# Performance work log

Hardware: AMD Instinct MI355X
Metric: run time of the kernel (lower is better)

Reference implementation:

```python
import jax, jax.numpy as jnp
from jax import lax
import numpy as np

S = 2048      # seq_len
E = 1024      # embedding_dim
H = 512       # hidden per direction (hidden_dim // 2)
V = 50000     # vocab
T = 16        # tagset_size
START, STOP = 0, 1
NEG = -10000.0


def setup_inputs() -> dict:
    key = jax.random.key(0)
    ks = jax.random.split(key, 20)
    bound = 1.0 / np.sqrt(H)

    def u(k, shape):
        return jax.random.uniform(k, shape, minval=-bound, maxval=bound, dtype=jnp.float32)

    sentence = jax.random.randint(ks[0], (S,), 0, V)
    emb = jax.random.normal(ks[1], (V, E), dtype=jnp.float32) * 0.1
    # PyTorch LSTM weights, gate order (i, f, g, o) stacked along first dim
    Wih_f = u(ks[2], (4 * H, E)); Whh_f = u(ks[3], (4 * H, H))
    bih_f = u(ks[4], (4 * H,));   bhh_f = u(ks[5], (4 * H,))
    Wih_b = u(ks[6], (4 * H, E)); Whh_b = u(ks[7], (4 * H, H))
    bih_b = u(ks[8], (4 * H,));   bhh_b = u(ks[9], (4 * H,))
    # init_hidden(): randn initial (h0, c0), [2 directions, H] (batch=1 squeezed)
    h0 = jax.random.normal(ks[10], (2, H), dtype=jnp.float32)
    c0 = jax.random.normal(ks[11], (2, H), dtype=jnp.float32)
    Wout = u(ks[12], (T, 2 * H)); bout = u(ks[13], (T,))
    transitions = jax.random.normal(ks[14], (T, T), dtype=jnp.float32)
    transitions = transitions.at[START, :].set(NEG).at[:, STOP].set(NEG)
    return dict(sentence=sentence, emb=emb,
                Wih_f=Wih_f, Whh_f=Whh_f, bih_f=bih_f, bhh_f=bhh_f,
                Wih_b=Wih_b, Whh_b=Whh_b, bih_b=bih_b, bhh_b=bhh_b,
                h0=h0, c0=c0, Wout=Wout, bout=bout, transitions=transitions)


def _lstm_dir(x, Wih, Whh, bih, bhh, h0, c0):
    # x: [S, E] -> hs: [S, H]; PyTorch gate order i, f, g, o
    xg = x @ Wih.T + bih + bhh  # precompute input contribution [S, 4H]

    def step(carry, xg_t):
        h, c = carry
        g = xg_t + h @ Whh.T
        i, f, gg, o = jnp.split(g, 4)
        i, f, o = jax.nn.sigmoid(i), jax.nn.sigmoid(f), jax.nn.sigmoid(o)
        c = f * c + i * jnp.tanh(gg)
        h = o * jnp.tanh(c)
        return (h, c), h

    _, hs = lax.scan(step, (h0, c0), xg)
    return hs


def _feats(sentence, emb, Wih_f, Whh_f, bih_f, bhh_f, Wih_b, Whh_b, bih_b, bhh_b,
           h0, c0, Wout, bout):
    x = emb[sentence]  # [S, E]
    hf = _lstm_dir(x, Wih_f, Whh_f, bih_f, bhh_f, h0[0], c0[0])              # [S, H]
    hb = _lstm_dir(x[::-1], Wih_b, Whh_b, bih_b, bhh_b, h0[1], c0[1])[::-1]  # [S, H]
    out = jnp.concatenate([hf, hb], axis=-1)  # [S, 2H]
    return out @ Wout.T + bout                # [S, T]


def _viterbi(feats, transitions):
    v0 = jnp.full((T,), NEG, dtype=feats.dtype).at[START].set(0.0)

    def vstep(v, feat):
        scores = v[None, :] + transitions        # [T(next), T(prev)]
        bp = jnp.argmax(scores, axis=1)          # best prev tag per next tag
        v_new = jnp.max(scores, axis=1) + feat
        return v_new, bp

    v, bps = lax.scan(vstep, v0, feats)          # bps: [S, T]
    terminal = v + transitions[STOP]
    best = jnp.argmax(terminal)
    path_score = terminal[best]

    def btstep(tag, bp):
        return bp[tag], tag

    _, path = lax.scan(btstep, best, bps, reverse=True)  # path[t] = tag at t
    return path_score, path


def reference(sentence, emb, Wih_f, Whh_f, bih_f, bhh_f, Wih_b, Whh_b, bih_b, bhh_b,
              h0, c0, Wout, bout, transitions):
    feats = _feats(sentence, emb, Wih_f, Whh_f, bih_f, bhh_f,
                   Wih_b, Whh_b, bih_b, bhh_b, h0, c0, Wout, bout)
    path_score, path = _viterbi(feats, transitions)
    return path_score, path
```

## Files before the change

kernel.cpp:

```cpp
#include <hip/hip_runtime.h>
#include <hip/hip_bf16.h>

#define S 2048
#define NEGV -10000.0f

typedef unsigned long long ull;
typedef unsigned int uint4v __attribute__((ext_vector_type(4)));

__device__ __forceinline__ float fsig(float x) {
  return 1.0f / (1.0f + __expf(-x));
}
__device__ __forceinline__ float ftanh(float x) {
  float a = fabsf(x);
  float e = __expf(-2.0f * a);
  float r = (1.0f - e) / (1.0f + e);
  return copysignf(r, x);
}

__global__ void init_k(const float* __restrict__ h0, ull* __restrict__ hbuf,
                       int* __restrict__ flags) {
  int b = blockIdx.x, u = threadIdx.x;
  if (b < 2) {
    ull pk = (1ULL << 32) | (ull)__float_as_uint(h0[b * 512 + u]);
    __hip_atomic_store(&hbuf[b * 1024 + u], pk, __ATOMIC_RELAXED, __HIP_MEMORY_SCOPE_AGENT);
    __hip_atomic_store(&hbuf[b * 1024 + 512 + u], 0ULL, __ATOMIC_RELAXED, __HIP_MEMORY_SCOPE_AGENT);
  } else {
    __hip_atomic_store(&flags[(b - 2) * 512 + u], 0, __ATOMIC_RELAXED, __HIP_MEMORY_SCOPE_AGENT);
    if (b == 2 && u < 2)
      __hip_atomic_store(&flags[2048 + u], 0, __ATOMIC_RELAXED, __HIP_MEMORY_SCOPE_AGENT);
  }
}

__device__ __forceinline__ ull compose_map(ull a, ull b) {
  ull r = 0;
  #pragma unroll
  for (int i = 0; i < 16; ++i) {
    int bi = (int)((b >> (4 * i)) & 15);
    int ai = (int)((a >> (4 * bi)) & 15);
    r |= (ull)ai << (4 * i);
  }
  return r;
}

__device__ __forceinline__ ull spread16(ull x) {
  x &= 0xFFFFULL;
  x = (x | (x << 24)) & 0x000000FF000000FFULL;
  x = (x | (x << 12)) & 0x000F000F000F000FULL;
  x = (x | (x << 6))  & 0x0303030303030303ULL;
  x = (x | (x << 3))  & 0x1111111111111111ULL;
  return x;
}

__global__ __launch_bounds__(256) void fused_k(
    const int* __restrict__ sent, const float* __restrict__ emb,
    const float* __restrict__ Wih_f, const float* __restrict__ Wih_b,
    const float* __restrict__ bih_f, const float* __restrict__ bhh_f,
    const float* __restrict__ bih_b, const float* __restrict__ bhh_b,
    const float* __restrict__ Whh_f, const float* __restrict__ Whh_b,
    const float* __restrict__ c0,
    const float* __restrict__ Wout, const float* __restrict__ bout,
    const float* __restrict__ trans,
    float* __restrict__ xg,
    ull* __restrict__ hbuf,
    float* __restrict__ hs_cat,
    float* __restrict__ feats,
    int* __restrict__ flags,
    float* __restrict__ out)
{
  __shared__ __align__(16) float smem[4544];
  const int t = threadIdx.x;

  if (blockIdx.x >= 128) {
    float* Asm = smem;
    float* Bsm = smem + 2304;
    int*   sidx = (int*)(smem + 4480);
    const int tm = t >> 4, tn = t & 15;
    const int lr = t >> 2, lkq = t & 3;

    for (int i = 0; i < 16; ++i) {
      const int T = (blockIdx.x - 128) + 128 * i;
      const int byo = T >> 6, bxo = T & 63;
      const int by = (byo & 1) ? (31 - (byo >> 1)) : (byo >> 1);
      const int bx = (bxo & 1) ? (32 + (bxo >> 1)) : (bxo >> 1);
      const int n0 = bx * 64, m0 = by * 64;

      const float* W = (n0 < 2048) ? (Wih_f + (size_t)n0 * 1024)
                                   : (Wih_b + (size_t)(n0 - 2048) * 1024);
      __syncthreads();
      if (t < 64) sidx[t] = sent[m0 + t];
      __syncthreads();

      float acc[4][4] = {};
      for (int k0 = 0; k0 < 1024; k0 += 32) {
        const float* ap = emb + (size_t)sidx[lr] * 1024 + k0 + lkq * 8;
        float4 a0 = *(const float4*)ap;
        float4 a1 = *(const float4*)(ap + 4);
        const float* bp = W + (size_t)lr * 1024 + k0 + lkq * 8;
        float4 b0 = *(const float4*)bp;
        float4 b1 = *(const float4*)(bp + 4);
        __syncthreads();
        *(float4*)&Asm[lr * 36 + lkq * 8]     = a0;
        *(float4*)&Asm[lr * 36 + lkq * 8 + 4] = a1;
        {
          const float* bb0 = (const float*)&b0;
          const float* bb1 = (const float*)&b1;
          #pragma unroll
          for (int j = 0; j < 4; ++j) Bsm[(lkq * 8 + j) * 68 + lr] = bb0[j];
          #pragma unroll
          for (int j = 0; j < 4; ++j) Bsm[(lkq * 8 + 4 + j) * 68 + lr] = bb1[j];
        }
        __syncthreads();
        #pragma unroll
        for (int kk = 0; kk < 32; ++kk) {
          float a0_ = Asm[(tm * 4 + 0) * 36 + kk];
          float a1_ = Asm[(tm * 4 + 1) * 36 + kk];
          float a2_ = Asm[(tm * 4 + 2) * 36 + kk];
          float a3_ = Asm[(tm * 4 + 3) * 36 + kk];
          float4 bv = *(const float4*)&Bsm[kk * 68 + tn * 4];
          acc[0][0] = fmaf(a0_, bv.x, acc[0][0]); acc[0][1] = fmaf(a0_, bv.y, acc[0][1]);
          acc[0][2] = fmaf(a0_, bv.z, acc[0][2]); acc[0][3] = fmaf(a0_, bv.w, acc[0][3]);
          acc[1][0] = fmaf(a1_, bv.x, acc[1][0]); acc[1][1] = fmaf(a1_, bv.y, acc[1][1]);
          acc[1][2] = fmaf(a1_, bv.z, acc[1][2]); acc[1][3] = fmaf(a1_, bv.w, acc[1][3]);
          acc[2][0] = fmaf(a2_, bv.x, acc[2][0]); acc[2][1] = fmaf(a2_, bv.y, acc[2][1]);
          acc[2][2] = fmaf(a2_, bv.z, acc[2][2]); acc[2][3] = fmaf(a2_, bv.w, acc[2][3]);
          acc[3][0] = fmaf(a3_, bv.x, acc[3][0]); acc[3][1] = fmaf(a3_, bv.y, acc[3][1]);
          acc[3][2] = fmaf(a3_, bv.z, acc[3][2]); acc[3][3] = fmaf(a3_, bv.w, acc[3][3]);
        }
      }

      const float* bi = (n0 < 2048) ? bih_f : bih_b;
      const float* bh = (n0 < 2048) ? bhh_f : bhh_b;
      const int nb = (n0 < 2048) ? n0 : (n0 - 2048);
      #pragma unroll
      for (int ii = 0; ii < 4; ++ii) {
        int m = m0 + tm * 4 + ii;
        #pragma unroll
        for (int j = 0; j < 4; ++j) {
          int nn = tn * 4 + j;
          float bias = bi[nb + nn] + bh[nb + nn];
          __hip_atomic_store(&xg[(size_t)m * 4096 + n0 + nn], acc[ii][j] + bias,
                             __ATOMIC_RELAXED, __HIP_MEMORY_SCOPE_AGENT);
        }
      }
      asm volatile("s_waitcnt vmcnt(0)" ::: "memory");
      __syncthreads();
      if (t == 0)
        __hip_atomic_store(&flags[by * 64 + bx], 1, __ATOMIC_RELAXED, __HIP_MEMORY_SCOPE_AGENT);
    }
    return;
  }

  {
    const int w = blockIdx.x;
    const int dir = w & 1;
    const int wid = w >> 1;
    const int rr = t >> 3;
    const int seg = t & 7;
    const int g  = rr & 3;
    const int ul = rr >> 2;
    const int unit = wid * 8 + ul;
    const int grow = g * 512 + unit;
    const int bxf  = dir * 32 + g * 8 + (wid >> 3);

    float (*h_lds)[544] = (float(*)[544])smem;

    const float* Whh = dir ? Whh_b : Whh_f;
    float wreg[64];
    {
      const float* src = Whh + (size_t)grow * 512 + seg * 64;
      #pragma unroll
      for (int j = 0; j < 16; ++j) {
        float4 v = *(const float4*)(src + j * 4);
        wreg[4 * j + 0] = v.x; wreg[4 * j + 1] = v.y;
        wreg[4 * j + 2] = v.z; wreg[4 * j + 3] = v.w;
      }
    }

    ull* hb = hbuf + dir * 1024;
    float c_reg = c0[dir * 512 + unit];

    const int u0 = t * 2;
    const int wchunk = u0 >> 6, wpos = u0 & 63;

    float xg_a = 0.0f, xg_b = 0.0f;
    if (seg == 0) {
      int by0 = dir ? 31 : 0;
      while (__hip_atomic_load(&flags[by0 * 64 + bxf], __ATOMIC_RELAXED,
                               __HIP_MEMORY_SCOPE_AGENT) != 1)
        __builtin_amdgcn_s_sleep(8);
      int r0 = dir ? (S - 1) : 0;
      int r1 = dir ? (S - 2) : 1;
      xg_a = __hip_atomic_load(&xg[(size_t)r0 * 4096 + dir * 2048 + grow],
                               __ATOMIC_RELAXED, __HIP_MEMORY_SCOPE_AGENT);
      xg_b = __hip_atomic_load(&xg[(size_t)r1 * 4096 + dir * 2048 + grow],
                               __ATOMIC_RELAXED, __HIP_MEMORY_SCOPE_AGENT);
    }

    #define LSTM_STEP(K, XG_REG)                                                  \
    {                                                                             \
      const int k = (K);                                                          \
      float xgv = XG_REG;                                                         \
      if (seg == 0 && k + 2 < S) {            \
        int rowk = dir ? (S - 3 - k) : (k + 2);                                   \
        if ((rowk & 63) == (dir ? 63 : 0)) {       \
          int byn = rowk >> 6;                                                    \
          while (__hip_atomic_load(&flags[byn * 64 + bxf], __ATOMIC_RELAXED,      \
                                   __HIP_MEMORY_SCOPE_AGENT) != 1)                \
            __builtin_amdgcn_s_sleep(8);                                          \
        }                                                                         \
        XG_REG = __hip_atomic_load(&xg[(size_t)rowk * 4096 + dir * 2048 + grow],  \
                                   __ATOMIC_RELAXED, __HIP_MEMORY_SCOPE_AGENT);   \
      }                                                                           \
           \
      {                                                                           \
        ull* src = hb + (k & 1) * 512 + u0;                                       \
        const unsigned want = (unsigned)(k + 1);                                  \
        uint4v v;                                                                 \
        asm volatile("global_load_dwordx4 %0, %1, off sc0 sc1"                    \
                     : "=v"(v) : "v"(src) : "memory");                            \
        asm volatile("s_waitcnt vmcnt(0)" ::: "memory");                          \
        while (v.y != want || v.w != want) {                                      \
          __builtin_amdgcn_s_sleep(1);                                            \
          asm volatile("global_load_dwordx4 %0, %1, off sc0 sc1"                  \
                       : "=v"(v) : "v"(src) : "memory");                          \
          asm volatile("s_waitcnt vmcnt(0)" ::: "memory");                        \
        }                                                                         \
        float* dst = &h_lds[k & 1][wchunk * 68 + wpos];                           \
        dst[0] = __uint_as_float(v.x);                                            \
        dst[1] = __uint_as_float(v.z);                                            \
      }                                                                           \
      __syncthreads();                                                            \
                                           \
      const float* hl = &h_lds[k & 1][0];                                         \
      float p0 = 0.f, p1 = 0.f, p2 = 0.f, p3 = 0.f;                               \
      const float4* h4 = (const float4*)(hl + seg * 68);                          \
      _Pragma("unroll")                                                           \
      for (int j = 0; j < 16; ++j) {                                              \
        float4 hv = h4[j];                                                        \
        p0 = fmaf(wreg[4 * j + 0], hv.x, p0);                                     \
        p1 = fmaf(wreg[4 * j + 1], hv.y, p1);                                     \
        p2 = fmaf(wreg[4 * j + 2], hv.z, p2);                                     \
        p3 = fmaf(wreg[4 * j + 3], hv.w, p3);                                     \
      }                                                                           \
      float p = (p0 + p1) + (p2 + p3) + xgv;                                      \
      p += __shfl_xor(p, 1);                                                      \
      p += __shfl_xor(p, 2);                                                      \
      p += __shfl_xor(p, 4);                                                      \
      float gb_ = __shfl_xor(p, 8);                                 \
      float gc_ = __shfl_xor(p, 16);                                \
      float gd_ = __shfl_xor(gb_, 16);                              \
      if (g == 0) {                                                               \
        float iv = fsig(p), fv = fsig(gb_), ov = fsig(gd_);                       \
        float gv = ftanh(gc_);                                                    \
        c_reg = fv * c_reg + iv * gv;                                             \
        float hv = ov * ftanh(c_reg);                                             \
        if (seg == 0) {                                                           \
          ull pk = ((ull)(unsigned)(k + 2) << 32) | (ull)__float_as_uint(hv);     \
          __hip_atomic_store(&hb[((k + 1) & 1) * 512 + unit], pk,                 \
                             __ATOMIC_RELAXED, __HIP_MEMORY_SCOPE_AGENT);         \
          int orig = dir ? (S - 1 - k) : k;                                       \
          hs_cat[(size_t)orig * 1024 + dir * 512 + unit] = hv;  \
        }                                                                         \
      }                                                                           \
    }

    for (int kk = 0; kk < S; kk += 2) {
      LSTM_STEP(kk, xg_a);
      LSTM_STEP(kk + 1, xg_b);
    }
    #undef LSTM_STEP

    asm volatile("s_waitcnt vmcnt(0)" ::: "memory");
    __syncthreads();
    {
      const int base = dir * 512 + wid * 8;
      for (int i = t; i < 16384; i += 256) {
        const int row = i >> 3, u2 = i & 7;
        float* p = &hs_cat[(size_t)row * 1024 + base + u2];
        float v = *p;
        __hip_atomic_store(p, v, __ATOMIC_RELAXED, __HIP_MEMORY_SCOPE_AGENT);
      }
    }
    asm volatile("s_waitcnt vmcnt(0)" ::: "memory");
    __syncthreads();
    if (t == 0)
      __hip_atomic_fetch_add(&flags[2048], 1, __ATOMIC_RELAXED, __HIP_MEMORY_SCOPE_AGENT);
  }

  if (t == 0) {
    while (__hip_atomic_load(&flags[2048], __ATOMIC_RELAXED,
                             __HIP_MEMORY_SCOPE_AGENT) != 128)
      __builtin_amdgcn_s_sleep(8);
  }
  __syncthreads();
  {
    const int l = t & 63;
    const int wv4 = t >> 6;
    const int j = l & 15, q = l >> 4;
    #pragma unroll
    for (int r = 0; r < 4; ++r) {
      const int tpos = blockIdx.x * 16 + wv4 * 4 + r;
      const float* h = hs_cat + (size_t)tpos * 1024 + q * 256;
      const float* wp = Wout + (size_t)j * 1024 + q * 256;
      float s = 0.f;
      #pragma unroll 8
      for (int i = 0; i < 256; i += 4) {
        float4 hv = *(const float4*)(h + i);
        float4 ww = *(const float4*)(wp + i);
        s = fmaf(hv.x, ww.x, s); s = fmaf(hv.y, ww.y, s);
        s = fmaf(hv.z, ww.z, s); s = fmaf(hv.w, ww.w, s);
      }
      s += __shfl_xor(s, 16);
      s += __shfl_xor(s, 32);
      if (q == 0)
        __hip_atomic_store(&feats[tpos * 16 + j], s + bout[j],
                           __ATOMIC_RELAXED, __HIP_MEMORY_SCOPE_AGENT);
    }
  }
  asm volatile("s_waitcnt vmcnt(0)" ::: "memory");
  __syncthreads();
  if (t == 0)
    __hip_atomic_fetch_add(&flags[2049], 1, __ATOMIC_RELAXED, __HIP_MEMORY_SCOPE_AGENT);

  if (blockIdx.x == 0) {
    if (t == 0) {
      while (__hip_atomic_load(&flags[2049], __ATOMIC_RELAXED,
                               __HIP_MEMORY_SCOPE_AGENT) != 128)
        __builtin_amdgcn_s_sleep(8);
    }
    __syncthreads();

    ull* bpm = (ull*)smem;
    const int l = t;
    float term; int ti;

    if (t < 64) {
      const int next = l & 15, q4 = (l >> 4) * 4;
      const float tr0 = trans[next * 16 + q4 + 0];
      const float tr1 = trans[next * 16 + q4 + 1];
      const float tr2 = trans[next * 16 + q4 + 2];
      const float tr3 = trans[next * 16 + q4 + 3];

      float vcur = (next == 0) ? 0.0f : NEGV;

      #define VSTEP(T, FREG)                                                    \
      {                                                                         \
        float pv0 = __shfl(vcur, q4 + 0, 16);                                   \
        float pv1 = __shfl(vcur, q4 + 1, 16);                                   \
        float pv2 = __shfl(vcur, q4 + 2, 16);                                   \
        float pv3 = __shfl(vcur, q4 + 3, 16);                                   \
        float m = pv0 + tr0; int mi = q4;                                       \
        float s1 = pv1 + tr1; if (s1 > m) { m = s1; mi = q4 + 1; }              \
        float s2 = pv2 + tr2; if (s2 > m) { m = s2; mi = q4 + 2; }              \
        float s3 = pv3 + tr3; if (s3 > m) { m = s3; mi = q4 + 3; }              \
        { float om = __shfl_xor(m, 16); int omi = __shfl_xor(mi, 16);           \
          if (om > m || (om == m && omi < mi)) { m = om; mi = omi; } }          \
        { float om = __shfl_xor(m, 32); int omi = __shfl_xor(mi, 32);           \
          if (om > m || (om == m && omi < mi)) { m = om; mi = omi; } }          \
        vcur = m + (FREG);                                                      \
        ull b0 = __ballot(mi & 1) & 0xFFFFULL;                                  \
        ull b1 = __ballot(mi & 2) & 0xFFFFULL;                                  \
        ull b2 = __ballot(mi & 4) & 0xFFFFULL;                                  \
        ull b3 = __ballot(mi & 8) & 0xFFFFULL;                                  \
        ull map = spread16(b0) | (spread16(b1) << 1) |                          \
                  (spread16(b2) << 2) | (spread16(b3) << 3);                    \
        if (l == 0) bpm[T] = map;                                               \
      }

      float f0 = feats[0 * 16 + next], f1 = feats[1 * 16 + next];
      float f2 = feats[2 * 16 + next], f3 = feats[3 * 16 + next];
      float f4 = feats[4 * 16 + next], f5 = feats[5 * 16 + next];
      float f6 = feats[6 * 16 + next], f7 = feats[7 * 16 + next];

      for (int tt = 0; tt < S; tt += 8) {
        VSTEP(tt + 0, f0); if (tt + 8  < S) f0 = feats[(tt + 8)  * 16 + next];
        VSTEP(tt + 1, f1); if (tt + 9  < S) f1 = feats[(tt + 9)  * 16 + next];
        VSTEP(tt + 2, f2); if (tt + 10 < S) f2 = feats[(tt + 10) * 16 + next];
        VSTEP(tt + 3, f3); if (tt + 11 < S) f3 = feats[(tt + 11) * 16 + next];
        VSTEP(tt + 4, f4); if (tt + 12 < S) f4 = feats[(tt + 12) * 16 + next];
        VSTEP(tt + 5, f5); if (tt + 13 < S) f5 = feats[(tt + 13) * 16 + next];
        VSTEP(tt + 6, f6); if (tt + 14 < S) f6 = feats[(tt + 14) * 16 + next];
        VSTEP(tt + 7, f7); if (tt + 15 < S) f7 = feats[(tt + 15) * 16 + next];
      }
      #undef VSTEP

      term = vcur + trans[16 + next];
      ti = next;
      #pragma unroll
      for (int mask = 1; mask <= 8; mask <<= 1) {
        float om = __shfl_xor(term, mask);
        int omi = __shfl_xor(ti, mask);
        if (om > term || (om == term && omi < ti)) { term = om; ti = omi; }
      }
    }

    __syncthreads();

    if (t < 64) {
      ull M = bpm[32 * l + 31];
      for (int i = 30; i >= 0; --i) M = compose_map(bpm[32 * l + i], M);
      ull Sm = M;
      #pragma unroll
      for (int d = 1; d < 64; d <<= 1) {
        ull o = __shfl_down(Sm, d);
        if (l + d < 64) Sm = compose_map(Sm, o);
      }
      ull G = __shfl_down(Sm, 1);
      if (l == 63) G = 0xFEDCBA9876543210ULL;

      int cur = (int)((G >> (4 * ti)) & 15);
      for (int i = 31; i >= 1; --i) {
        int tt = 32 * l + i;
        out[1 + tt] = (float)cur;
        cur = (int)((bpm[tt] >> (4 * cur)) & 15);
      }
      out[1 + 32 * l] = (float)cur;
      if (l == 0) out[0] = term;
    }
  }
}

extern "C" void kernel_launch(void* const* d_in, const int* in_sizes, int n_in,
                              void* d_out, int out_size, void* d_ws, size_t ws_size,
                              hipStream_t stream) {
  const int*   sent  = (const int*)d_in[0];
  const float* emb   = (const float*)d_in[1];
  const float* Wih_f = (const float*)d_in[2];
  const float* Whh_f = (const float*)d_in[3];
  const float* bih_f = (const float*)d_in[4];
  const float* bhh_f = (const float*)d_in[5];
  const float* Wih_b = (const float*)d_in[6];
  const float* Whh_b = (const float*)d_in[7];
  const float* bih_b = (const float*)d_in[8];
  const float* bhh_b = (const float*)d_in[9];
  const float* h0    = (const float*)d_in[10];
  const float* c0    = (const float*)d_in[11];
  const float* Wout  = (const float*)d_in[12];
  const float* bout  = (const float*)d_in[13];
  const float* trans = (const float*)d_in[14];
  float* out = (float*)d_out;

  char* ws = (char*)d_ws;
  float* xg     = (float*)(ws);
  float* hs_cat = (float*)(ws + 33554432);
  float* feats  = (float*)(ws + 41943040);
  ull*   hbuf   = (ull*)  (ws + 42074112);
  int*   flags  = (int*)  (ws + 42090496);

  init_k<<<6, 512, 0, stream>>>(h0, hbuf, flags);
  fused_k<<<256, 256, 0, stream>>>(sent, emb, Wih_f, Wih_b, bih_f, bhh_f,
                                   bih_b, bhh_b, Whh_f, Whh_b, c0, Wout, bout,
                                   trans, xg, hbuf, hs_cat, feats, flags, out);
}
```

Baseline: 3.967 ms.

## Parallelize Viterbi forward pass via chunked max-plus matrix products

Replaces the serial 2048-step Viterbi recurrence in block 0 with a three-phase scheme. First, 16 groups each build max-plus transfer matrices for 64-step chunks in parallel. Then a short serial scan over 32 chunk matrices produces the boundary score vectors, and each chunk is recomputed in parallel from its boundary to record byte backpointers. It shortens the serial critical path of the tail stage, at the cost of roughly 16x more max-plus arithmetic, more shared memory, and possible tie-breaking differences from reassociated max.

```diff
diff --git a/kernel.cpp b/kernel.cpp
--- a/kernel.cpp
+++ b/kernel.cpp
@@ -40,15 +40,6 @@
     r |= (ull)ai << (4 * i);
   }
   return r;
-}
-
-__device__ __forceinline__ ull spread16(ull x) {
-  x &= 0xFFFFULL;
-  x = (x | (x << 24)) & 0x000000FF000000FFULL;
-  x = (x | (x << 12)) & 0x000F000F000F000FULL;
-  x = (x | (x << 6))  & 0x0303030303030303ULL;
-  x = (x | (x << 3))  & 0x1111111111111111ULL;
-  return x;
 }
 
 __global__ __launch_bounds__(256) void fused_k(
@@ -67,7 +58,7 @@
     int* __restrict__ flags,
     float* __restrict__ out)
 {
-  __shared__ __align__(16) float smem[4544];
+  __shared__ __align__(16) float smem[9232];
   const int t = threadIdx.x;
 
   if (blockIdx.x >= 128) {
@@ -330,92 +321,168 @@
     }
     __syncthreads();
 
-    ull* bpm = (ull*)smem;
-    const int l = t;
-    float term; int ti;
-
-    if (t < 64) {
-      const int next = l & 15, q4 = (l >> 4) * 4;
-      const float tr0 = trans[next * 16 + q4 + 0];
-      const float tr1 = trans[next * 16 + q4 + 1];
-      const float tr2 = trans[next * 16 + q4 + 2];
-      const float tr3 = trans[next * 16 + q4 + 3];
-
-      float vcur = (next == 0) ? 0.0f : NEGV;
-
-      #define VSTEP(T, FREG)                                                    \
-      {                                                                         \
-        float pv0 = __shfl(vcur, q4 + 0, 16);                                   \
-        float pv1 = __shfl(vcur, q4 + 1, 16);                                   \
-        float pv2 = __shfl(vcur, q4 + 2, 16);                                   \
-        float pv3 = __shfl(vcur, q4 + 3, 16);                                   \
-        float m = pv0 + tr0; int mi = q4;                                       \
-        float s1 = pv1 + tr1; if (s1 > m) { m = s1; mi = q4 + 1; }              \
-        float s2 = pv2 + tr2; if (s2 > m) { m = s2; mi = q4 + 2; }              \
-        float s3 = pv3 + tr3; if (s3 > m) { m = s3; mi = q4 + 3; }              \
-        { float om = __shfl_xor(m, 16); int omi = __shfl_xor(mi, 16);           \
-          if (om > m || (om == m && omi < mi)) { m = om; mi = omi; } }          \
-        { float om = __shfl_xor(m, 32); int omi = __shfl_xor(mi, 32);           \
-          if (om > m || (om == m && omi < mi)) { m = om; mi = omi; } }          \
-        vcur = m + (FREG);                                                      \
-        ull b0 = __ballot(mi & 1) & 0xFFFFULL;                                  \
-        ull b1 = __ballot(mi & 2) & 0xFFFFULL;                                  \
-        ull b2 = __ballot(mi & 4) & 0xFFFFULL;                                  \
-        ull b3 = __ballot(mi & 8) & 0xFFFFULL;                                  \
-        ull map = spread16(b0) | (spread16(b1) << 1) |                          \
-                  (spread16(b2) << 2) | (spread16(b3) << 3);                    \
-        if (l == 0) bpm[T] = map;                                               \
-      }
-
-      float f0 = feats[0 * 16 + next], f1 = feats[1 * 16 + next];
-      float f2 = feats[2 * 16 + next], f3 = feats[3 * 16 + next];
-      float f4 = feats[4 * 16 + next], f5 = feats[5 * 16 + next];
-      float f6 = feats[6 * 16 + next], f7 = feats[7 * 16 + next];
-
-      for (int tt = 0; tt < S; tt += 8) {
-        VSTEP(tt + 0, f0); if (tt + 8  < S) f0 = feats[(tt + 8)  * 16 + next];
-        VSTEP(tt + 1, f1); if (tt + 9  < S) f1 = feats[(tt + 9)  * 16 + next];
-        VSTEP(tt + 2, f2); if (tt + 10 < S) f2 = feats[(tt + 10) * 16 + next];
-        VSTEP(tt + 3, f3); if (tt + 11 < S) f3 = feats[(tt + 11) * 16 + next];
-        VSTEP(tt + 4, f4); if (tt + 12 < S) f4 = feats[(tt + 12) * 16 + next];
-        VSTEP(tt + 5, f5); if (tt + 13 < S) f5 = feats[(tt + 13) * 16 + next];
-        VSTEP(tt + 6, f6); if (tt + 14 < S) f6 = feats[(tt + 14) * 16 + next];
-        VSTEP(tt + 7, f7); if (tt + 15 < S) f7 = feats[(tt + 15) * 16 + next];
-      }
-      #undef VSTEP
-
-      term = vcur + trans[16 + next];
-      ti = next;
+    float* P_ls  = smem;
+    float* vb    = smem + 8192;
+    float* Trows = smem + 8704;
+    float* vg    = smem + 8960;
+    float* tslot = smem + 9216;
+
+    if (t < 256) Trows[t] = trans[t];
+    __syncthreads();
+
+    const int G = t >> 4, r = t & 15;
+
+    {
+      float Tcol[16];
+      #pragma unroll
+      for (int j = 0; j < 16; ++j) Tcol[j] = Trows[j * 16 + r];
+
+      for (int cc = 0; cc < 2; ++cc) {
+        const int c = G * 2 + cc, t0 = c * 64;
+        float P[16];
+        {
+          const float4* fr = (const float4*)&feats[t0 * 16];
+          float4 fA = fr[0], fB = fr[1], fC = fr[2], fD = fr[3];
+          float ff[16];
+          ff[0]=fA.x; ff[1]=fA.y; ff[2]=fA.z; ff[3]=fA.w;
+          ff[4]=fB.x; ff[5]=fB.y; ff[6]=fB.z; ff[7]=fB.w;
+          ff[8]=fC.x; ff[9]=fC.y; ff[10]=fC.z; ff[11]=fC.w;
+          ff[12]=fD.x; ff[13]=fD.y; ff[14]=fD.z; ff[15]=fD.w;
+          #pragma unroll
+          for (int j = 0; j < 16; ++j) P[j] = Tcol[j] + ff[j];
+        }
+        for (int tt = t0 + 1; tt < t0 + 64; ++tt) {
+          const float4* fr = (const float4*)&feats[tt * 16];
+          float4 fA = fr[0], fB = fr[1], fC = fr[2], fD = fr[3];
+          float ff[16];
+          ff[0]=fA.x; ff[1]=fA.y; ff[2]=fA.z; ff[3]=fA.w;
+          ff[4]=fB.x; ff[5]=fB.y; ff[6]=fB.z; ff[7]=fB.w;
+          ff[8]=fC.x; ff[9]=fC.y; ff[10]=fC.z; ff[11]=fC.w;
+          ff[12]=fD.x; ff[13]=fD.y; ff[14]=fD.z; ff[15]=fD.w;
+          float Q[16];
+          #pragma unroll
+          for (int j = 0; j < 16; ++j) {
+            const float4 Ta = *(const float4*)&Trows[j * 16 + 0];
+            const float4 Tb = *(const float4*)&Trows[j * 16 + 4];
+            const float4 Tc2 = *(const float4*)&Trows[j * 16 + 8];
+            const float4 Td = *(const float4*)&Trows[j * 16 + 12];
+            float m0 = fmaxf(P[0]  + Ta.x,  P[1]  + Ta.y);
+            float m1 = fmaxf(P[2]  + Ta.z,  P[3]  + Ta.w);
+            float m2 = fmaxf(P[4]  + Tb.x,  P[5]  + Tb.y);
+            float m3 = fmaxf(P[6]  + Tb.z,  P[7]  + Tb.w);
+            float m4 = fmaxf(P[8]  + Tc2.x, P[9]  + Tc2.y);
+            float m5 = fmaxf(P[10] + Tc2.z, P[11] + Tc2.w);
+            float m6 = fmaxf(P[12] + Td.x,  P[13] + Td.y);
+            float m7 = fmaxf(P[14] + Td.z,  P[15] + Td.w);
+            float m = fmaxf(fmaxf(fmaxf(m0, m1), fmaxf(m2, m3)),
+                            fmaxf(fmaxf(m4, m5), fmaxf(m6, m7)));
+            Q[j] = m + ff[j];
+          }
+          #pragma unroll
+          for (int j = 0; j < 16; ++j) P[j] = Q[j];
+        }
+        #pragma unroll
+        for (int j = 0; j < 16; ++j) P_ls[c * 256 + r * 16 + j] = P[j];
+      }
+    }
+    __syncthreads();
+
+    if (t < 16) {
+      float m = (t == 0) ? 0.0f : NEGV;
+      for (int c = 0; c < 32; ++c) {
+        float vv[16];
+        #pragma unroll
+        for (int i = 0; i < 16; ++i) vv[i] = __shfl(m, i, 16);
+        float nm = vv[0] + P_ls[c * 256 + 0 * 16 + t];
+        #pragma unroll
+        for (int i = 1; i < 16; ++i)
+          nm = fmaxf(nm, vv[i] + P_ls[c * 256 + i * 16 + t]);
+        vb[c * 16 + t] = nm;
+        m = nm;
+      }
+    }
+    __syncthreads();
+
+    {
+      unsigned char* bpB = (unsigned char*)P_ls;
+      float Trow[16];
+      #pragma unroll
+      for (int k2 = 0; k2 < 16; ++k2) Trow[k2] = Trows[r * 16 + k2];
+
+      for (int cc = 0; cc < 2; ++cc) {
+        const int c = G * 2 + cc, t0 = c * 64;
+        float vcur = (c == 0) ? ((r == 0) ? 0.0f : NEGV) : vb[(c - 1) * 16 + r];
+        float fnext = feats[t0 * 16 + r];
+        for (int tt = t0; tt < t0 + 64; ++tt) {
+          float f = fnext;
+          if (tt + 1 < t0 + 64) fnext = feats[(tt + 1) * 16 + r];
+          float vv[16];
+          #pragma unroll
+          for (int i = 0; i < 16; ++i) vv[i] = __shfl(vcur, i, 16);
+          float m = vv[0] + Trow[0]; int mi = 0;
+          #pragma unroll
+          for (int i = 1; i < 16; ++i) {
+            float s2 = vv[i] + Trow[i];
+            if (s2 > m) { m = s2; mi = i; }
+          }
+          vcur = m + f;
+          bpB[tt * 16 + r] = (unsigned char)mi;
+        }
+      }
+    }
+    __syncthreads();
+
+    if (t < 16) {
+      float term = vb[31 * 16 + t] + trans[16 + t];
+      int ti = t;
       #pragma unroll
       for (int mask = 1; mask <= 8; mask <<= 1) {
         float om = __shfl_xor(term, mask);
         int omi = __shfl_xor(ti, mask);
         if (om > term || (om == term && omi < ti)) { term = om; ti = omi; }
       }
-    }
-
+      if (t == 0) { tslot[0] = term; tslot[1] = __int_as_float(ti); }
+    }
     __syncthreads();
 
     if (t < 64) {
-      ull M = bpm[32 * l + 31];
-      for (int i = 30; i >= 0; --i) M = compose_map(bpm[32 * l + i], M);
+      const unsigned char* bpB = (const unsigned char*)P_ls;
+      const int l = t;
+      ull M = 0;
+      {
+        const int tb = 32 * l + 31;
+        #pragma unroll
+        for (int j = 0; j < 16; ++j)
+          M |= (ull)(bpB[tb * 16 + j] & 15) << (4 * j);
+      }
+      for (int i = 30; i >= 0; --i) {
+        const int ta = 32 * l + i;
+        ull Mn = 0;
+        #pragma unroll
+        for (int j = 0; j < 16; ++j) {
+          int idx = (int)((M >> (4 * j)) & 15);
+          Mn |= (ull)(bpB[ta * 16 + idx] & 15) << (4 * j);
+        }
+        M = Mn;
+      }
       ull Sm = M;
       #pragma unroll
       for (int d = 1; d < 64; d <<= 1) {
         ull o = __shfl_down(Sm, d);
         if (l + d < 64) Sm = compose_map(Sm, o);
       }
-      ull G = __shfl_down(Sm, 1);
-      if (l == 63) G = 0xFEDCBA9876543210ULL;
-
-      int cur = (int)((G >> (4 * ti)) & 15);
+      ull Gm = __shfl_down(Sm, 1);
+      if (l == 63) Gm = 0xFEDCBA9876543210ULL;
+
+      int ti = __float_as_int(tslot[1]);
+      int cur = (int)((Gm >> (4 * ti)) & 15);
       for (int i = 31; i >= 1; --i) {
-        int tt = 32 * l + i;
-        out[1 + tt] = (float)cur;
-        cur = (int)((bpm[tt] >> (4 * cur)) & 15);
+        int tt2 = 32 * l + i;
+        out[1 + tt2] = (float)cur;
+        cur = bpB[tt2 * 16 + cur] & 15;
       }
       out[1 + 32 * l] = (float)cur;
-      if (l == 0) out[0] = term;
+      if (l == 0) out[0] = tslot[0];
     }
   }
 }
```

After: 3.474 ms. 12.4% less time.
